# Performance work log

Hardware: AMD Instinct MI355X
Metric: run time of the kernel (lower is better)

## Reference

```python
import jax, jax.numpy as jnp
import numpy as np

N = 4_000_000   # nodes
C = 8           # classes
K = 8192        # number of complexes (segments)
ALPHA = 0.5     # weight on per-complex sum(=mean*len) vs max
GAMMA = 2.0     # focal focusing parameter


def setup_inputs() -> dict:
    key = jax.random.key(0)
    k1, k2, k3 = jax.random.split(key, 3)
    logits = jax.random.normal(k1, (N, C), dtype=jnp.float32)
    targets = jax.random.randint(k2, (N,), 0, C)
    complex_id = jnp.sort(jax.random.randint(k3, (N,), 0, K))
    return {"logits": logits, "targets": targets, "complex_id": complex_id}


def reference(logits, targets, complex_id):
    # per-node cross entropy (reduction='none', weight=None)
    logp = jax.nn.log_softmax(logits, axis=-1)                    # [N, C]
    ce = -jnp.take_along_axis(logp, targets[:, None], axis=-1)[:, 0]  # [N]
    # focal weighting: (1 - exp(-ce))**gamma * ce
    pt = jnp.exp(-ce)
    node_loss = (1.0 - pt) ** GAMMA * ce                          # [N]

    # fused segment reduction: sum (== mean * len), max, and counts per complex
    seg_sum = jax.ops.segment_sum(node_loss, complex_id, num_segments=K,
                                  indices_are_sorted=True)        # [K]
    seg_max = jax.ops.segment_max(node_loss, complex_id, num_segments=K,
                                  indices_are_sorted=True)        # [K] (-inf for empty)
    counts = jax.ops.segment_sum(jnp.ones_like(node_loss), complex_id,
                                 num_segments=K, indices_are_sorted=True)  # [K]
    present = counts > 0

    complex_loss = ALPHA * seg_sum + (1.0 - ALPHA) * jnp.where(present, seg_max, 0.0)
    n_present = jnp.maximum(jnp.sum(present.astype(jnp.float32)), 1.0)
    return jnp.sum(jnp.where(present, complex_loss, 0.0)) / n_present
```

## Files before the change

kernel.cpp:

```cpp
#include <hip/hip_runtime.h>

#define K_SEGS 8192
#define ALPHA_W 0.5f
#define NEG_INF_BITS 0xFF800000
#define WIN 64
#define NBLOCKS 2048
#define BLOCK 256
#define SHARD_SZ 32
#define NSHARDS (NBLOCKS / SHARD_SZ)

#define SHARD_BASE (3 * K_SEGS)
#define STAGE2_OFF (SHARD_BASE + NSHARDS * 16)
#define WS_WORDS (STAGE2_OFF + 16)

__global__ void init_ws_kernel(unsigned* __restrict__ w) {
    int i = blockIdx.x * blockDim.x + threadIdx.x;
    if (i < WS_WORDS) w[i] = 0u;
}

__device__ __forceinline__ float node_focal(float4 a, float4 b, int t) {
    float x0 = a.x, x1 = a.y, x2 = a.z, x3 = a.w;
    float x4 = b.x, x5 = b.y, x6 = b.z, x7 = b.w;
    float m = fmaxf(fmaxf(fmaxf(x0, x1), fmaxf(x2, x3)),
                    fmaxf(fmaxf(x4, x5), fmaxf(x6, x7)));
    float s = __expf(x0 - m) + __expf(x1 - m) + __expf(x2 - m) + __expf(x3 - m)
            + __expf(x4 - m) + __expf(x5 - m) + __expf(x6 - m) + __expf(x7 - m);
    float lse = __logf(s) + m;
    float xt;
    switch (t) {
        case 0: xt = x0; break; case 1: xt = x1; break;
        case 2: xt = x2; break; case 3: xt = x3; break;
        case 4: xt = x4; break; case 5: xt = x5; break;
        case 6: xt = x6; break; default: xt = x7; break;
    }
    float ce = lse - xt;
    float pt = __expf(-ce);
    float om = 1.0f - pt;
    return om * om * ce;
}

__global__ __launch_bounds__(BLOCK) void node_loss_kernel(
        const float* __restrict__ logits,
        const int* __restrict__ targets,
        const int* __restrict__ cid,
        float* __restrict__ seg_sum,
        unsigned* __restrict__ seg_maxb,
        unsigned* __restrict__ seg_cnt,
        unsigned* __restrict__ shard_tk,
        unsigned* __restrict__ stage2_tk,
        float* __restrict__ out,
        int n) {
    __shared__ float lsum[WIN];
    __shared__ int   lmax[WIN];
    __shared__ unsigned s_last;
    __shared__ float s_fa[4], s_fn[4];

    const int tid  = threadIdx.x;
    const int lane = tid & 63;

    const int chunk  = (n + NBLOCKS - 1) / NBLOCKS;
    const int cstart = blockIdx.x * chunk;

    if (cstart < n) {
        const int cend = min(cstart + chunk, n);
        const int base = cid[cstart];

        for (int j = tid; j < WIN; j += BLOCK) {
            lsum[j] = 0.0f;
            lmax[j] = (int)NEG_INF_BITS;
        }
        __syncthreads();

        for (int i0 = cstart + tid * 2; __any(i0 < cend); i0 += BLOCK * 2) {
            bool v0 = (i0 < cend);
            bool v1 = (i0 + 1 < cend);
            float la = 0.0f, lb = 0.0f;
            int offa = -1, offb = -2;
            if (v0) {
                const float4* lg = reinterpret_cast<const float4*>(logits) + (size_t)i0 * 2;
                float4 a0 = lg[0];
                float4 a1 = lg[1];
                float4 b0, b1;
                int ta, tb = 0;
                if (v1) {
                    b0 = lg[2];
                    b1 = lg[3];
                    int2 tt = *reinterpret_cast<const int2*>(targets + i0);
                    int2 cc = *reinterpret_cast<const int2*>(cid + i0);
                    ta = tt.x; tb = tt.y;
                    offa = cc.x - base;
                    offb = cc.y - base;
                } else {
                    ta = targets[i0];
                    offa = cid[i0] - base;
                }
                la = node_focal(a0, a1, ta);
                if (v1) lb = node_focal(b0, b1, tb);
            }

            int u = __shfl(offa, 0);
            bool uniform = __all(offa == u && offb == u) && (u < WIN);
            if (uniform) {
                float tsum = la + lb;
                float tmax = fmaxf(la, lb);
                #pragma unroll
                for (int o = 32; o > 0; o >>= 1) {
                    tsum += __shfl_xor(tsum, o);
                    tmax = fmaxf(tmax, __shfl_xor(tmax, o));
                }
                if (lane == 0) {
                    atomicAdd(&lsum[u], tsum);
                    atomicMax(&lmax[u], __float_as_int(tmax));
                }
            } else {
                if (v0) {
                    if (offa < WIN) {
                        atomicAdd(&lsum[offa], la);
                        atomicMax(&lmax[offa], __float_as_int(la));
                    } else {
                        atomicAdd(&seg_sum[base + offa], la);
                        atomicMax(&seg_maxb[base + offa], __float_as_uint(la));
                        atomicAdd(&seg_cnt[base + offa], 1u);
                    }
                }
                if (v1) {
                    if (offb < WIN) {
                        atomicAdd(&lsum[offb], lb);
                        atomicMax(&lmax[offb], __float_as_int(lb));
                    } else {
                        atomicAdd(&seg_sum[base + offb], lb);
                        atomicMax(&seg_maxb[base + offb], __float_as_uint(lb));
                        atomicAdd(&seg_cnt[base + offb], 1u);
                    }
                }
            }
        }
        __syncthreads();

        for (int j = tid; j < WIN; j += BLOCK) {
            int mb = lmax[j];
            if (mb != (int)NEG_INF_BITS) {
                atomicAdd(&seg_sum[base + j], lsum[j]);
                atomicMax(&seg_maxb[base + j], (unsigned)mb);
                atomicAdd(&seg_cnt[base + j], 1u);
            }
        }
    }

    asm volatile("s_waitcnt vmcnt(0)" ::: "memory");
    __syncthreads();
    if (tid == 0) {
        unsigned fin = 0u;
        unsigned my = atomicAdd(&shard_tk[(blockIdx.x / SHARD_SZ) * 16], 1u);
        if (my == (unsigned)(SHARD_SZ - 1)) {
            fin = atomicAdd(&stage2_tk[0], 1u) + 1u;
        }
        s_last = (fin == (unsigned)NSHARDS) ? 1u : 0u;
    }
    __syncthreads();
    if (s_last) {
        float acc = 0.0f, np = 0.0f;
        #pragma unroll 8
        for (int k = tid; k < K_SEGS; k += BLOCK) {
            unsigned c = __hip_atomic_load(&seg_cnt[k],  __ATOMIC_RELAXED, __HIP_MEMORY_SCOPE_AGENT);
            float s    = __hip_atomic_load(&seg_sum[k],  __ATOMIC_RELAXED, __HIP_MEMORY_SCOPE_AGENT);
            unsigned m = __hip_atomic_load(&seg_maxb[k], __ATOMIC_RELAXED, __HIP_MEMORY_SCOPE_AGENT);
            if (c != 0u) {
                acc += ALPHA_W * s + (1.0f - ALPHA_W) * __uint_as_float(m);
                np += 1.0f;
            }
        }
        #pragma unroll
        for (int o = 32; o > 0; o >>= 1) {
            acc += __shfl_xor(acc, o);
            np  += __shfl_xor(np, o);
        }
        if (lane == 0) { s_fa[tid >> 6] = acc; s_fn[tid >> 6] = np; }
        __syncthreads();
        if (tid == 0) {
            float a = s_fa[0] + s_fa[1] + s_fa[2] + s_fa[3];
            float c = s_fn[0] + s_fn[1] + s_fn[2] + s_fn[3];
            out[0] = a / fmaxf(c, 1.0f);
        }
    }
}

extern "C" void kernel_launch(void* const* d_in, const int* in_sizes, int n_in,
                              void* d_out, int out_size, void* d_ws, size_t ws_size,
                              hipStream_t stream) {
    const float* logits = (const float*)d_in[0];
    const int* targets  = (const int*)d_in[1];
    const int* cid      = (const int*)d_in[2];
    float* out          = (float*)d_out;

    const int n = in_sizes[1];

    unsigned* w        = (unsigned*)d_ws;
    float* seg_sum     = (float*)w;
    unsigned* seg_maxb = w + K_SEGS;
    unsigned* seg_cnt  = w + 2 * K_SEGS;
    unsigned* shard_tk = w + SHARD_BASE;
    unsigned* stage2_tk= w + STAGE2_OFF;

    init_ws_kernel<<<(WS_WORDS + 255) / 256, 256, 0, stream>>>(w);

    node_loss_kernel<<<NBLOCKS, BLOCK, 0, stream>>>(logits, targets, cid,
                                                    seg_sum, seg_maxb, seg_cnt,
                                                    shard_tk, stage2_tk, out, n);
}
```

Baseline: 41.64 us.

## Split each node's logits across lane pairs with fully coalesced float4 loads

Each wave now processes 128 consecutive nodes, with two lanes per node each loading one float4, so consecutive lanes read contiguous memory. Max, sum-exp and target selection are combined across the lane pair with shuffles. Segment uniformity is decided from the first and last cid of the window instead of a wave vote. This targets load coalescing for the bandwidth-bound logits read, at the cost of extra shuffles and duplicated loss values that the uniform path halves.

Result: slower. 43.54 us (+4.6%).

```diff
diff --git a/kernel.cpp b/kernel.cpp
--- a/kernel.cpp
+++ b/kernel.cpp
@@ -18,27 +18,6 @@
     if (i < WS_WORDS) w[i] = 0u;
 }
 
-__device__ __forceinline__ float node_focal(float4 a, float4 b, int t) {
-    float x0 = a.x, x1 = a.y, x2 = a.z, x3 = a.w;
-    float x4 = b.x, x5 = b.y, x6 = b.z, x7 = b.w;
-    float m = fmaxf(fmaxf(fmaxf(x0, x1), fmaxf(x2, x3)),
-                    fmaxf(fmaxf(x4, x5), fmaxf(x6, x7)));
-    float s = __expf(x0 - m) + __expf(x1 - m) + __expf(x2 - m) + __expf(x3 - m)
-            + __expf(x4 - m) + __expf(x5 - m) + __expf(x6 - m) + __expf(x7 - m);
-    float lse = __logf(s) + m;
-    float xt;
-    switch (t) {
-        case 0: xt = x0; break; case 1: xt = x1; break;
-        case 2: xt = x2; break; case 3: xt = x3; break;
-        case 4: xt = x4; break; case 5: xt = x5; break;
-        case 6: xt = x6; break; default: xt = x7; break;
-    }
-    float ce = lse - xt;
-    float pt = __expf(-ce);
-    float om = 1.0f - pt;
-    return om * om * ce;
-}
-
 __global__ __launch_bounds__(BLOCK) void node_loss_kernel(
         const float* __restrict__ logits,
         const int* __restrict__ targets,
@@ -57,6 +36,7 @@
 
     const int tid  = threadIdx.x;
     const int lane = tid & 63;
+    const int wv   = tid >> 6;
 
     const int chunk  = (n + NBLOCKS - 1) / NBLOCKS;
     const int cstart = blockIdx.x * chunk;
@@ -71,66 +51,73 @@
         }
         __syncthreads();
 
-        for (int i0 = cstart + tid * 2; __any(i0 < cend); i0 += BLOCK * 2) {
-            bool v0 = (i0 < cend);
-            bool v1 = (i0 + 1 < cend);
-            float la = 0.0f, lb = 0.0f;
-            int offa = -1, offb = -2;
-            if (v0) {
-                const float4* lg = reinterpret_cast<const float4*>(logits) + (size_t)i0 * 2;
-                float4 a0 = lg[0];
-                float4 a1 = lg[1];
-                float4 b0, b1;
-                int ta, tb = 0;
-                if (v1) {
-                    b0 = lg[2];
-                    b1 = lg[3];
-                    int2 tt = *reinterpret_cast<const int2*>(targets + i0);
-                    int2 cc = *reinterpret_cast<const int2*>(cid + i0);
-                    ta = tt.x; tb = tt.y;
-                    offa = cc.x - base;
-                    offb = cc.y - base;
-                } else {
-                    ta = targets[i0];
-                    offa = cid[i0] - base;
-                }
-                la = node_focal(a0, a1, ta);
-                if (v1) lb = node_focal(b0, b1, tb);
+        const float4* lgf = reinterpret_cast<const float4*>(logits);
+
+        for (int wstart = cstart + wv * 128; wstart < cend; wstart += BLOCK * 2) {
+            const int wlast = min(wstart + 127, cend - 1);
+            const int ufirst = cid[wstart];
+            const int ulast  = cid[wlast];
+            const int ubase  = ufirst - base;
+            const bool uniform = (ufirst == ulast) && (ubase < WIN);
+
+            float loss[4];
+            #pragma unroll
+            for (int j = 0; j < 4; ++j) {
+                const int h = j * 64 + lane;
+                const int node = wstart + (h >> 1);
+                const bool v = (node < cend);
+                float4 x;
+                if (v) x = lgf[(size_t)wstart * 2 + h];
+                else   x = make_float4(0.f, 0.f, 0.f, 0.f);
+
+                float m4 = fmaxf(fmaxf(x.x, x.y), fmaxf(x.z, x.w));
+                float m8 = fmaxf(m4, __shfl_xor(m4, 1));
+                float s4 = __expf(x.x - m8) + __expf(x.y - m8)
+                         + __expf(x.z - m8) + __expf(x.w - m8);
+                float s8 = s4 + __shfl_xor(s4, 1);
+                float lse = __logf(s8) + m8;
+
+                int t = v ? targets[node] : 0;
+                float xsel = (t & 2) ? ((t & 1) ? x.w : x.z)
+                                     : ((t & 1) ? x.y : x.x);
+                float xc = ((t >> 2) == (lane & 1)) ? xsel : -1e30f;
+                float xt = fmaxf(xc, __shfl_xor(xc, 1));
+
+                float ce = lse - xt;
+                float pt = __expf(-ce);
+                float om = 1.0f - pt;
+                loss[j] = v ? om * om * ce : 0.0f;
             }
 
-            int u = __shfl(offa, 0);
-            bool uniform = __all(offa == u && offb == u) && (u < WIN);
             if (uniform) {
-                float tsum = la + lb;
-                float tmax = fmaxf(la, lb);
+                float tsum = (loss[0] + loss[1]) + (loss[2] + loss[3]);
+                float tmax = fmaxf(fmaxf(loss[0], loss[1]), fmaxf(loss[2], loss[3]));
                 #pragma unroll
                 for (int o = 32; o > 0; o >>= 1) {
                     tsum += __shfl_xor(tsum, o);
                     tmax = fmaxf(tmax, __shfl_xor(tmax, o));
                 }
                 if (lane == 0) {
-                    atomicAdd(&lsum[u], tsum);
-                    atomicMax(&lmax[u], __float_as_int(tmax));
+                    atomicAdd(&lsum[ubase], 0.5f * tsum);
+                    atomicMax(&lmax[ubase], __float_as_int(tmax));
                 }
             } else {
-                if (v0) {
-                    if (offa < WIN) {
-                        atomicAdd(&lsum[offa], la);
-                        atomicMax(&lmax[offa], __float_as_int(la));
-                    } else {
-                        atomicAdd(&seg_sum[base + offa], la);
-                        atomicMax(&seg_maxb[base + offa], __float_as_uint(la));
-                        atomicAdd(&seg_cnt[base + offa], 1u);
-                    }
-                }
-                if (v1) {
-                    if (offb < WIN) {
-                        atomicAdd(&lsum[offb], lb);
-                        atomicMax(&lmax[offb], __float_as_int(lb));
-                    } else {
-                        atomicAdd(&seg_sum[base + offb], lb);
-                        atomicMax(&seg_maxb[base + offb], __float_as_uint(lb));
-                        atomicAdd(&seg_cnt[base + offb], 1u);
+                if ((lane & 1) == 0) {
+                    #pragma unroll
+                    for (int j = 0; j < 4; ++j) {
+                        const int node = wstart + j * 32 + (lane >> 1);
+                        if (node < cend) {
+                            const int cn = cid[node];
+                            const int off = cn - base;
+                            if (off < WIN) {
+                                atomicAdd(&lsum[off], loss[j]);
+                                atomicMax(&lmax[off], __float_as_int(loss[j]));
+                            } else {
+                                atomicAdd(&seg_sum[cn], loss[j]);
+                                atomicMax(&seg_maxb[cn], __float_as_uint(loss[j]));
+                                atomicAdd(&seg_cnt[cn], 1u);
+                            }
+                        }
                     }
                 }
             }
```
